# Kernel optimization log

Hardware: AMD Instinct MI355X
Metric: run time of the kernel (lower is better)

The kernel has to match this reference:

```python
import jax, jax.numpy as jnp
import numpy as np

B, N, K, F, S = 128, 116, 4, 72, 8
TOPK = 10
INTRA_T, INTER_T = 0.1, 0.2


def _safe_corr(f):
    # f: [batch, d, m] -> corr [batch, d, d], matching torch _safe_compute_correlation
    c = f - f.mean(axis=2, keepdims=True)
    cov = jnp.einsum('bim,bjm->bij', c, c)
    var = jnp.diagonal(cov, axis1=1, axis2=2)
    std = jnp.sqrt(jnp.clip(var, 1e-8, None))[:, :, None]
    corr = cov / (std * std.transpose(0, 2, 1) + 1e-8)
    return jnp.clip(corr, -1.0, 1.0)


def _sym(m):
    return (m + m.swapaxes(-1, -2)) * 0.5


def setup_inputs():
    key = jax.random.key(0)
    ks = jax.random.split(key, 8)
    def lin(k, out_d, in_d):
        return jax.random.normal(k, (out_d, in_d), jnp.float32) * (1.0 / np.sqrt(in_d))
    return {
        'band_features': jax.random.normal(ks[0], (B, N, K, F), jnp.float32),
        'attn_weights': jax.random.uniform(ks[1], (B, N, S, K), jnp.float32),
        'intra_thresh_adj': jnp.zeros((), jnp.float32),
        'inter_thresh_adj': jnp.zeros((), jnp.float32),
        'attn_fuse_weight': jnp.asarray(0.5, jnp.float32),
        'intra_W1': lin(ks[2], 64, N), 'intra_b1': jnp.zeros((64,), jnp.float32),
        'intra_W2': lin(ks[3], N, 64), 'intra_b2': jnp.zeros((N,), jnp.float32),
        'inter_W1': lin(ks[4], 32, K), 'inter_b1': jnp.zeros((32,), jnp.float32),
        'inter_W2': lin(ks[5], K, 32), 'inter_b2': jnp.zeros((K,), jnp.float32),
        'comp_W': lin(ks[6], 128, 2 * F + 6), 'comp_b': jnp.zeros((128,), jnp.float32),
    }


def reference(band_features, attn_weights, intra_thresh_adj, inter_thresh_adj,
              attn_fuse_weight, intra_W1, intra_b1, intra_W2, intra_b2,
              inter_W1, inter_b1, inter_W2, inter_b2, comp_W, comp_b):
    dt = band_features.dtype
    # ---- intra-band graph: [B*K, N, N] correlations ----
    x = band_features.transpose(0, 2, 1, 3).reshape(B * K, N, F)
    corr = _safe_corr(x)
    th = INTRA_T + jax.nn.sigmoid(intra_thresh_adj) * 0.2
    tmask = (jnp.abs(corr) > th).astype(dt)
    _, idx = jax.lax.top_k(jnp.abs(corr), min(TOPK, N))  # [B*K, N, k]
    bix = jnp.arange(B * K)[:, None, None]
    rix = jnp.arange(N)[None, :, None]
    kmask = jnp.zeros_like(corr).at[bix, rix, idx].set(1.0)
    sc = jax.nn.relu(_sym(corr * tmask * kmask))
    h = jax.nn.relu(sc.reshape(-1, N) @ intra_W1.T + intra_b1)  # dropout = eval identity
    intra = jax.nn.sigmoid(h @ intra_W2.T + intra_b2).reshape(B * K, N, N)
    intra_adj = _sym(intra).reshape(B, K, N, N)
    # ---- inter-band graph: [B*N, K, K] correlations ----
    y = band_features.reshape(B * N, K, F)
    base = _safe_corr(y)
    a = attn_weights.reshape(B * N, S, K).transpose(0, 2, 1)  # [B*N, K, S]
    acorr = _safe_corr(a)
    fw = jax.nn.sigmoid(attn_fuse_weight)
    base = fw * base + (1.0 - fw) * acorr
    th2 = INTER_T + jax.nn.sigmoid(inter_thresh_adj) * 0.2
    sc2 = jax.nn.relu(_sym(base * (jnp.abs(base) > th2).astype(dt)))
    h2 = jax.nn.relu(sc2.reshape(-1, K) @ inter_W1.T + inter_b1)
    inter = jax.nn.sigmoid(h2 @ inter_W2.T + inter_b2).reshape(B * N, K, K)
    inter_adj = _sym(inter).reshape(B, N, K, K)
    # ---- unified graph assembly (vectorized replacement of nested loops) ----
    kk = jnp.arange(K)
    bd = jnp.zeros((B, K, N, K, N), dt).at[:, kk, :, kk, :].set(
        intra_adj.transpose(1, 0, 2, 3))  # block-diagonal intra blocks
    unified = bd.reshape(B, K * N, K * N)
    kk1, kk2, nn = np.meshgrid(np.arange(K), np.arange(K), np.arange(N), indexing='ij')
    sel = (kk1 != kk2).ravel()
    k1f, k2f, nf = kk1.ravel()[sel], kk2.ravel()[sel], nn.ravel()[sel]
    vals = inter_adj[:, nf, k1f, k2f]  # [B, M]
    unified_adj = unified.at[:, k1f * N + nf, k2f * N + nf].set(vals)
    # ---- node features ----
    node_features = band_features.transpose(0, 2, 1, 3).reshape(B, K * N, F)
    # ---- graph-level features ----
    node_mean = band_features.mean(axis=(1, 2))
    node_std = jnp.std(band_features, axis=(1, 2), ddof=1)  # torch unbiased std
    deg = (intra_adj > 0).astype(dt).sum(axis=3)  # [B, K, N]
    tri = jnp.einsum('bkij,bkji->bki', intra_adj, intra_adj)  # diag of A@A
    clus = tri / (deg ** 2 + 1e-8)
    dens = (inter_adj > 0).astype(dt).mean(axis=(2, 3))  # [B, N]
    stren = inter_adj.mean(axis=(2, 3))
    gf = jnp.concatenate([
        node_mean, node_std,
        deg.mean(axis=(1, 2))[:, None], jnp.std(deg, axis=(1, 2), ddof=1)[:, None],
        clus.mean(axis=(1, 2))[:, None], jnp.std(clus, axis=(1, 2), ddof=1)[:, None],
        dens.mean(axis=1)[:, None], stren.mean(axis=1)[:, None]], axis=1)
    graph_features = jax.nn.relu(gf @ comp_W.T + comp_b)
    # ---- sparsity scalars ----
    intra_sp = 1.0 - (intra_adj > 0).astype(dt).mean()
    inter_sp = 1.0 - (inter_adj > 0).astype(dt).mean()
    it, jt = float(B * K * N * N), float(B * N * K * K)
    total_sp = (intra_sp * it + inter_sp * jt) / (it + jt)
    return (unified_adj, node_features, graph_features, intra_adj, inter_adj,
            intra_sp, inter_sp, total_sp)
```

## Files before the change

### kernel.cpp

```cpp
#include <hip/hip_runtime.h>
#include <math.h>

#define NB 128
#define NN_ 116
#define NK 4
#define NF 72
#define NS 8
#define TOPK 10

#define BK (NB*NK)
#define BN (NB*NN_)
#define NN2 (NN_*NN_)
#define KN (NK*NN_)
#define ROWS (BK*NN_)
#define LROW 117

#define OFF_UNI 0
#define SZ_UNI (NB*KN*KN)
#define OFF_NF (OFF_UNI + SZ_UNI)
#define SZ_NF (NB*KN*NF)
#define OFF_GF (OFF_NF + SZ_NF)
#define SZ_GF (NB*128)
#define OFF_IA (OFF_GF + SZ_GF)
#define SZ_IA (NB*NK*NN_*NN_)
#define OFF_IE (OFF_IA + SZ_IA)
#define SZ_IE (NB*NN_*NK*NK)
#define OFF_SP (OFF_IE + SZ_IE)

#define SCR_SC 0
#define SCR_CORR (SCR_SC + SZ_IA)
#define SCR_DEG (SCR_CORR + SZ_IA)
#define SCR_CLUS (SCR_DEG + ROWS)
#define SCR_DENS (SCR_CLUS + ROWS)
#define SCR_STREN (SCR_DENS + BN)
#define SCR_AUX (SCR_STREN + BN)

__device__ __forceinline__ float sigmoidf_(float x){ return 1.0f/(1.0f+expf(-x)); }
__device__ __forceinline__ float dot4_(float4 a, float4 b){
    return fmaf(a.x,b.x, fmaf(a.y,b.y, fmaf(a.z,b.z, a.w*b.w)));
}
#define CLIP1(x) fminf(1.0f, fmaxf(-1.0f, (x)))

__global__ __launch_bounds__(256, 1) void k_corr_inter(const float* __restrict__ band,
    const float* __restrict__ attn, const float* __restrict__ thadj2,
    const float* __restrict__ fwp,
    const float* __restrict__ eW1, const float* __restrict__ eb1,
    const float* __restrict__ eW2, const float* __restrict__ eb2,
    float* __restrict__ corr_out, float* __restrict__ inter_out,
    float* __restrict__ dens_out, float* __restrict__ stren_out)
{
    __shared__ float sx[NF*120];
    __shared__ float smu[120], srs[120];
    __shared__ float sW1[128], sb1[32], sW2[128], sb2[4];
    __shared__ float sMat[256*4];
    int t = threadIdx.x;
    if (blockIdx.x < 512){
        int bk = blockIdx.x;
        int b = bk >> 2, k = bk & 3;
        const float* xin = band + ((size_t)b*NN_*NK + k)*NF;
        for (int e = t; e < NN_*NF; e += 256){
            int n = e / NF, f = e - n*NF;
            sx[f*120 + n] = xin[(size_t)n*NK*NF + f];
        }
        for (int e = t; e < NF*4; e += 256)
            sx[(e>>2)*120 + NN_ + (e&3)] = 0.0f;
        __syncthreads();
        if (t < NN_){
            float s = 0.f, ss = 0.f;
            for (int f = 0; f < NF; ++f){ float v = sx[f*120+t]; s += v; ss += v*v; }
            float mu = s * (1.0f/NF);
            float sd = sqrtf(fmaxf(ss - s*mu, 1e-8f));
            smu[t] = mu; srs[t] = 1.0f/sd;
        }
        __syncthreads();
        for (int e = t; e < NF*NN_; e += 256){
            int f = e / NN_, n = e - f*NN_;
            sx[f*120+n] = (sx[f*120+n] - smu[n]) * srs[n];
        }
        __syncthreads();
        float* dst = corr_out + (size_t)bk * NN2;
        if (t < 225){
            int ti = t / 15, tj = t - ti*15;
            int i0 = ti*8, j0 = tj*8;
            float acc[8][8] = {};
            for (int f = 0; f < NF; ++f){
                const float4 a0 = *(const float4*)&sx[f*120 + i0];
                const float4 a1 = *(const float4*)&sx[f*120 + i0 + 4];
                const float4 c0 = *(const float4*)&sx[f*120 + j0];
                const float4 c1 = *(const float4*)&sx[f*120 + j0 + 4];
                float av[8] = {a0.x,a0.y,a0.z,a0.w,a1.x,a1.y,a1.z,a1.w};
                float cv[8] = {c0.x,c0.y,c0.z,c0.w,c1.x,c1.y,c1.z,c1.w};
                #pragma unroll
                for (int r = 0; r < 8; ++r)
                    #pragma unroll
                    for (int c = 0; c < 8; ++c)
                        acc[r][c] = fmaf(av[r], cv[c], acc[r][c]);
            }
            #pragma unroll
            for (int r = 0; r < 8; ++r){
                int i = i0 + r;
                if (i < NN_){
                    float4 v0;
                    v0.x = CLIP1(acc[r][0]); v0.y = CLIP1(acc[r][1]);
                    v0.z = CLIP1(acc[r][2]); v0.w = CLIP1(acc[r][3]);
                    *(float4*)&dst[i*NN_ + j0] = v0;
                    if (j0 + 4 <= 112){
                        float4 v1;
                        v1.x = CLIP1(acc[r][4]); v1.y = CLIP1(acc[r][5]);
                        v1.z = CLIP1(acc[r][6]); v1.w = CLIP1(acc[r][7]);
                        *(float4*)&dst[i*NN_ + j0 + 4] = v1;
                    }
                }
            }
        }
    } else {
        if (t < 128) sW1[t] = eW1[t];
        if (t < 32) sb1[t] = eb1[t];
        if (t >= 128 && t < 256) sW2[t-128] = eW2[t-128];
        if (t < 4) sb2[t] = eb2[t];
        __syncthreads();
        int l = t & 3;
        int il = t >> 2;
        size_t item = (size_t)(blockIdx.x - 512)*64 + il;

        const float* xr = band + item*(NK*NF) + l*NF;
        float s=0,p0=0,p1=0,p2=0,p3=0;
        for (int f = 0; f < NF; ++f){
            float v = xr[f];
            float v1=__shfl_xor(v,1), v2=__shfl_xor(v,2), v3=__shfl_xor(v,3);
            s += v; p0=fmaf(v,v,p0); p1=fmaf(v,v1,p1); p2=fmaf(v,v2,p2); p3=fmaf(v,v3,p3);
        }
        float mu = s*(1.0f/NF);
        float mu1=__shfl_xor(mu,1), mu2=__shfl_xor(mu,2), mu3=__shfl_xor(mu,3);
        float sd = sqrtf(fmaxf(p0 - s*mu, 1e-8f));
        float sd1=__shfl_xor(sd,1), sd2=__shfl_xor(sd,2), sd3=__shfl_xor(sd,3);
        float c0 = CLIP1((p0 - (float)NF*mu*mu )/(sd*sd +1e-8f));
        float c1 = CLIP1((p1 - (float)NF*mu*mu1)/(sd*sd1+1e-8f));
        float c2 = CLIP1((p2 - (float)NF*mu*mu2)/(sd*sd2+1e-8f));
        float c3 = CLIP1((p3 - (float)NF*mu*mu3)/(sd*sd3+1e-8f));

        const float* ar = attn + item*(NS*NK) + l;
        float as=0,q0=0,q1=0,q2=0,q3=0;
        #pragma unroll
        for (int s8 = 0; s8 < NS; ++s8){
            float v = ar[s8*NK];
            float v1=__shfl_xor(v,1), v2=__shfl_xor(v,2), v3=__shfl_xor(v,3);
            as += v; q0=fmaf(v,v,q0); q1=fmaf(v,v1,q1); q2=fmaf(v,v2,q2); q3=fmaf(v,v3,q3);
        }
        float am = as*(1.0f/NS);
        float am1=__shfl_xor(am,1), am2=__shfl_xor(am,2), am3=__shfl_xor(am,3);
        float ad = sqrtf(fmaxf(q0 - as*am, 1e-8f));
        float ad1=__shfl_xor(ad,1), ad2=__shfl_xor(ad,2), ad3=__shfl_xor(ad,3);
        float a0 = CLIP1((q0 - (float)NS*am*am )/(ad*ad +1e-8f));
        float a1 = CLIP1((q1 - (float)NS*am*am1)/(ad*ad1+1e-8f));
        float a2 = CLIP1((q2 - (float)NS*am*am2)/(ad*ad2+1e-8f));
        float a3 = CLIP1((q3 - (float)NS*am*am3)/(ad*ad3+1e-8f));

        float fwv = sigmoidf_(fwp[0]);
        float g0 = fwv*c0 + (1.0f-fwv)*a0;
        float g1 = fwv*c1 + (1.0f-fwv)*a1;
        float g2 = fwv*c2 + (1.0f-fwv)*a2;
        float g3 = fwv*c3 + (1.0f-fwv)*a3;
        float th2 = 0.2f + sigmoidf_(thadj2[0])*0.2f;
        float m0 = (fabsf(g0)>th2)?g0:0.f;
        float m1 = (fabsf(g1)>th2)?g1:0.f;
        float m2 = (fabsf(g2)>th2)?g2:0.f;
        float m3 = (fabsf(g3)>th2)?g3:0.f;

        sMat[il*16 + l*4 + (l^0)] = m0;
        sMat[il*16 + l*4 + (l^1)] = m1;
        sMat[il*16 + l*4 + (l^2)] = m2;
        sMat[il*16 + l*4 + (l^3)] = m3;
        __syncthreads();
        float x0 = fmaxf(0.5f*(sMat[il*16 + l*4 + 0] + sMat[il*16 + 0*4 + l]), 0.f);
        float x1 = fmaxf(0.5f*(sMat[il*16 + l*4 + 1] + sMat[il*16 + 1*4 + l]), 0.f);
        float x2 = fmaxf(0.5f*(sMat[il*16 + l*4 + 2] + sMat[il*16 + 2*4 + l]), 0.f);
        float x3 = fmaxf(0.5f*(sMat[il*16 + l*4 + 3] + sMat[il*16 + 3*4 + l]), 0.f);

        float h[32];
        #pragma unroll
        for (int o = 0; o < 32; ++o){
            float acc = sb1[o];
            acc = fmaf(sW1[o*4+0], x0, acc);
            acc = fmaf(sW1[o*4+1], x1, acc);
            acc = fmaf(sW1[o*4+2], x2, acc);
            acc = fmaf(sW1[o*4+3], x3, acc);
            h[o] = fmaxf(acc, 0.f);
        }
        float o0=sb2[0], o1=sb2[1], o2=sb2[2], o3=sb2[3];
        #pragma unroll
        for (int o = 0; o < 32; ++o){
            float hv = h[o];
            o0 = fmaf(sW2[0*32+o], hv, o0);
            o1 = fmaf(sW2[1*32+o], hv, o1);
            o2 = fmaf(sW2[2*32+o], hv, o2);
            o3 = fmaf(sW2[3*32+o], hv, o3);
        }
        o0 = sigmoidf_(o0); o1 = sigmoidf_(o1); o2 = sigmoidf_(o2); o3 = sigmoidf_(o3);
        __syncthreads();
        sMat[il*16 + l*4 + 0] = o0;
        sMat[il*16 + l*4 + 1] = o1;
        sMat[il*16 + l*4 + 2] = o2;
        sMat[il*16 + l*4 + 3] = o3;
        __syncthreads();
        float y0 = 0.5f*(o0 + sMat[il*16 + 0*4 + l]);
        float y1 = 0.5f*(o1 + sMat[il*16 + 1*4 + l]);
        float y2 = 0.5f*(o2 + sMat[il*16 + 2*4 + l]);
        float y3 = 0.5f*(o3 + sMat[il*16 + 3*4 + l]);
        *(float4*)&inter_out[item*16 + l*4] = make_float4(y0,y1,y2,y3);

        float cnt = ((y0>0.f)?1.f:0.f) + ((y1>0.f)?1.f:0.f) + ((y2>0.f)?1.f:0.f) + ((y3>0.f)?1.f:0.f);
        float sum = y0+y1+y2+y3;
        cnt += __shfl_xor(cnt,1); cnt += __shfl_xor(cnt,2);
        sum += __shfl_xor(sum,1); sum += __shfl_xor(sum,2);
        if (l == 0){
            dens_out[item]  = cnt * (1.0f/16.0f);
            stren_out[item] = sum * (1.0f/16.0f);
        }
    }
}

__global__ __launch_bounds__(512) void k_topk_mask(const float* __restrict__ corr_in,
    const float* __restrict__ thadj, float* __restrict__ sc_out)
{
    __shared__ float sc_[NN_*LROW];
    __shared__ unsigned skm[NN_*4];
    __shared__ unsigned stop[464*10];
    int bk = blockIdx.x;
    int t = threadIdx.x;
    const float* src = corr_in + (size_t)bk*NN2;
    for (int e = t; e < NN2; e += 512){
        int i = e / NN_, j = e - i*NN_;
        sc_[i*LROW + j] = src[e];
    }
    __syncthreads();
    if (t < NN_*4){
        int r = t >> 2, q = t & 3;
        const float* row = &sc_[r*LROW + q*29];
        int jbase = q*29;
        unsigned tv[TOPK];
        #pragma unroll
        for (int p = 0; p < TOPK; ++p) tv[p] = 0u;
        for (int jj = 0; jj < 29; ++jj){
            float c = fabsf(row[jj]);
            unsigned u = (__float_as_uint(c) & 0xFFFFFF80u) | (unsigned)(127 - (jbase + jj));
            #pragma unroll
            for (int p = 0; p < TOPK; ++p){
                unsigned old = tv[p];
                bool gt = u > old;
                tv[p] = gt ? u : old;
                u = gt ? old : u;
            }
        }
        #pragma unroll
        for (int p = 0; p < TOPK; ++p) stop[t*10 + p] = tv[p];
    }
    __syncthreads();
    if (t < NN_){
        const unsigned* L0 = &stop[(4*t+0)*10];
        const unsigned* L1 = &stop[(4*t+1)*10];
        const unsigned* L2 = &stop[(4*t+2)*10];
        const unsigned* L3 = &stop[(4*t+3)*10];
        int i0=0, i1=0, i2=0, i3=0;
        unsigned m0=0,m1=0,m2=0,m3=0;
        #pragma unroll
        for (int p = 0; p < TOPK; ++p){
            unsigned u0 = L0[i0], u1 = L1[i1], u2 = L2[i2], u3 = L3[i3];
            unsigned ua = u0 > u1 ? u0 : u1;
            unsigned ub = u2 > u3 ? u2 : u3;
            unsigned u  = ua > ub ? ua : ub;
            if (u == u0) ++i0; else if (u == u1) ++i1; else if (u == u2) ++i2; else ++i3;
            int j = 127 - (int)(u & 127u);
            unsigned bit = 1u << (j & 31);
            int w = j >> 5;
            if (w == 0) m0 |= bit; else if (w == 1) m1 |= bit; else if (w == 2) m2 |= bit; else m3 |= bit;
        }
        skm[t*4+0]=m0; skm[t*4+1]=m1; skm[t*4+2]=m2; skm[t*4+3]=m3;
    }
    __syncthreads();
    float th = 0.1f + sigmoidf_(thadj[0]) * 0.2f;
    float* dst = sc_out + (size_t)bk * NN2;
    for (int e = t; e < NN2; e += 512){
        int i = e / NN_, j = e - i*NN_;
        float cij = sc_[i*LROW + j];
        float cji = sc_[j*LROW + i];
        bool kij = (skm[i*4 + (j>>5)] >> (j&31)) & 1u;
        bool kji = (skm[j*4 + (i>>5)] >> (i&31)) & 1u;
        float mij = (fabsf(cij) > th && kij) ? cij : 0.0f;
        float mji = (fabsf(cji) > th && kji) ? cji : 0.0f;
        dst[e] = fmaxf(0.5f*(mij+mji), 0.0f);
    }
}

__global__ __launch_bounds__(256) void k_mlp(const float* __restrict__ sc,
    const float* __restrict__ W1, const float* __restrict__ b1,
    const float* __restrict__ W2, const float* __restrict__ b2,
    float* __restrict__ intra)
{
    __shared__ float sA_[14848];
    __shared__ float sH[64*68];
    __shared__ float sb1[64];
    __shared__ float sb2[128];
    int t = threadIdx.x;
    int r0 = blockIdx.x * 64;
    float* srow = sA_;
    float* sW1  = sA_ + 7424;
    for (int e4 = t; e4 < 1856; e4 += 256){
        *(float4*)&srow[e4*4] = *(const float4*)&sc[(size_t)r0*116 + e4*4];
        *(float4*)&sW1[e4*4]  = *(const float4*)&W1[e4*4];
    }
    if (t < 64) sb1[t] = b1[t];
    if (t < 128) sb2[t] = (t < NN_) ? b2[t] : 0.0f;
    __syncthreads();
    {
        int rg = t >> 4, og = t & 15;
        float acc[4][4] = {};
        for (int j4 = 0; j4 < 29; ++j4){
            float4 s[4], w[4];
            #pragma unroll
            for (int m = 0; m < 4; ++m) s[m] = *(const float4*)&srow[(rg+16*m)*116 + j4*4];
            #pragma unroll
            for (int n = 0; n < 4; ++n) w[n] = *(const float4*)&sW1[(og+16*n)*116 + j4*4];
            #pragma unroll
            for (int m = 0; m < 4; ++m)
                #pragma unroll
                for (int n = 0; n < 4; ++n)
                    acc[m][n] += dot4_(s[m], w[n]);
        }
        #pragma unroll
        for (int m = 0; m < 4; ++m)
            #pragma unroll
            for (int n = 0; n < 4; ++n)
                sH[(rg+16*m)*68 + og+16*n] = fmaxf(acc[m][n] + sb1[og+16*n], 0.0f);
    }
    __syncthreads();
    float* sW2 = sA_;
    for (int e = t; e < 128*64; e += 256){
        int j = e >> 6, o = e & 63;
        sW2[j*76 + o] = (j < NN_) ? W2[e] : 0.0f;
    }
    __syncthreads();
    {
        int rg = t >> 4, jg = t & 15;
        float acc[4][8] = {};
        for (int o4 = 0; o4 < 16; ++o4){
            float4 h[4], w[8];
            #pragma unroll
            for (int m = 0; m < 4; ++m) h[m] = *(const float4*)&sH[(rg+16*m)*68 + o4*4];
            #pragma unroll
            for (int q = 0; q < 8; ++q) w[q] = *(const float4*)&sW2[(jg+16*q)*76 + o4*4];
            #pragma unroll
            for (int m = 0; m < 4; ++m)
                #pragma unroll
                for (int q = 0; q < 8; ++q)
                    acc[m][q] += dot4_(h[m], w[q]);
        }
        #pragma unroll
        for (int m = 0; m < 4; ++m){
            int row = r0 + rg + 16*m;
            #pragma unroll
            for (int q = 0; q < 8; ++q){
                int j = jg + 16*q;
                if (j < NN_)
                    intra[(size_t)row*116 + j] = sigmoidf_(acc[m][q] + sb2[j]);
            }
        }
    }
}

__global__ __launch_bounds__(512) void k_sym_intra(const float* __restrict__ intra,
    float* __restrict__ intra_adj, float* __restrict__ deg_out, float* __restrict__ clus_out)
{
    __shared__ float sm[NN_*LROW];
    int bk = blockIdx.x, t = threadIdx.x;
    const float* src = intra + (size_t)bk*NN2;
    for (int e = t; e < NN2; e += 512){
        int i = e / NN_, j = e - i*NN_;
        sm[i*LROW + j] = src[e];
    }
    __syncthreads();
    float* dst = intra_adj + (size_t)bk*NN2;
    for (int e = t; e < NN2; e += 512){
        int i = e / NN_, j = e - i*NN_;
        dst[e] = 0.5f*(sm[i*LROW + j] + sm[j*LROW + i]);
    }
    if (t < NN_*4){
        int r = t >> 2, q = t & 3;
        float tri = 0.f, dg = 0.f;
        for (int jj = 0; jj < 29; ++jj){
            int j = q*29 + jj;
            float v = 0.5f*(sm[r*LROW+j] + sm[j*LROW+r]);
            tri = fmaf(v, v, tri);
            dg += (v > 0.f) ? 1.f : 0.f;
        }
        tri += __shfl_xor(tri,1); tri += __shfl_xor(tri,2);
        dg  += __shfl_xor(dg,1);  dg  += __shfl_xor(dg,2);
        if (q == 0){
            deg_out[(size_t)bk*NN_ + r]  = dg;
            clus_out[(size_t)bk*NN_ + r] = tri / (dg*dg + 1e-8f);
        }
    }
}

__global__ __launch_bounds__(256) void k_gstats_lin(const float* __restrict__ band,
    const float* __restrict__ deg, const float* __restrict__ clus,
    const float* __restrict__ dens, const float* __restrict__ stren,
    const float* __restrict__ Wc, const float* __restrict__ bc,
    float* __restrict__ gfo, float* __restrict__ aux)
{
    int b = blockIdx.x, t = threadIdx.x;
    __shared__ float sGf[152];
    __shared__ float sPs[18*14*4];
    __shared__ float sPq[18*14*4];
    __shared__ float sA[4], sB[4];

    if (t < 252){
        int fq = t % 18, g = t / 18;
        float4 s = make_float4(0,0,0,0), q = make_float4(0,0,0,0);
        const float* base = band + (size_t)b*(KN*NF);
        for (int nk = g; nk < KN; nk += 14){
            float4 v = *(const float4*)&base[nk*NF + fq*4];
            s.x += v.x; s.y += v.y; s.z += v.z; s.w += v.w;
            q.x = fmaf(v.x,v.x,q.x); q.y = fmaf(v.y,v.y,q.y);
            q.z = fmaf(v.z,v.z,q.z); q.w = fmaf(v.w,v.w,q.w);
        }
        int idx = (fq*14 + g)*4;
        *(float4*)&sPs[idx] = s;
        *(float4*)&sPq[idx] = q;
    }
    __syncthreads();
    if (t < NF){
        int fq = t >> 2, e = t & 3;
        float S = 0.f, Q = 0.f;
        for (int g = 0; g < 14; ++g){ S += sPs[(fq*14+g)*4+e]; Q += sPq[(fq*14+g)*4+e]; }
        float mean = S * (1.0f/(float)KN);
        float var = fmaxf((Q - S*mean)/((float)KN - 1.0f), 0.0f);
        sGf[t] = mean;
        sGf[NF + t] = sqrtf(var);
    }
    __syncthreads();

    float s = 0.f, ss = 0.f;
    for (int e = t; e < KN; e += 256){ float v = deg[(size_t)b*KN + e]; s += v; ss += v*v; }
    #pragma unroll
    for (int d = 1; d < 64; d <<= 1){ s += __shfl_xor(s,d); ss += __shfl_xor(ss,d); }
    if ((t & 63) == 0){ sA[t>>6] = s; sB[t>>6] = ss; }
    __syncthreads();
    if (t == 0){
        float S0 = sA[0]+sA[1]+sA[2]+sA[3], S1 = sB[0]+sB[1]+sB[2]+sB[3];
        float Mv = (float)KN, mean = S0/Mv;
        float var = fmaxf((S1 - S0*mean)/(Mv - 1.0f), 0.0f);
        sGf[144] = mean; sGf[145] = sqrtf(var);
        aux[b] = S0;
    }
    __syncthreads();

    s = 0.f; ss = 0.f;
    for (int e = t; e < KN; e += 256){ float v = clus[(size_t)b*KN + e]; s += v; ss += v*v; }
    #pragma unroll
    for (int d = 1; d < 64; d <<= 1){ s += __shfl_xor(s,d); ss += __shfl_xor(ss,d); }
    if ((t & 63) == 0){ sA[t>>6] = s; sB[t>>6] = ss; }
    __syncthreads();
    if (t == 0){
        float S0 = sA[0]+sA[1]+sA[2]+sA[3], S1 = sB[0]+sB[1]+sB[2]+sB[3];
        float Mv = (float)KN, mean = S0/Mv;
        float var = fmaxf((S1 - S0*mean)/(Mv - 1.0f), 0.0f);
        sGf[146] = mean; sGf[147] = sqrtf(var);
    }
    __syncthreads();

    s = 0.f; ss = 0.f;
    for (int e = t; e < NN_; e += 256){ s += dens[(size_t)b*NN_ + e]; ss += stren[(size_t)b*NN_ + e]; }
    #pragma unroll
    for (int d = 1; d < 64; d <<= 1){ s += __shfl_xor(s,d); ss += __shfl_xor(ss,d); }
    if ((t & 63) == 0){ sA[t>>6] = s; sB[t>>6] = ss; }
    __syncthreads();
    if (t == 0){
        float S0 = sA[0]+sA[1]+sA[2]+sA[3], S1 = sB[0]+sB[1]+sB[2]+sB[3];
        sGf[148] = S0 / (float)NN_;
        sGf[149] = S1 / (float)NN_;
        aux[128 + b] = S0 * 16.0f;
    }
    __syncthreads();

    if (t < 128){
        float acc = bc[t];
        const float* w = Wc + (size_t)t*150;
        for (int c = 0; c < 150; ++c) acc = fmaf(sGf[c], w[c], acc);
        gfo[(size_t)b*128 + t] = fmaxf(acc, 0.f);
    }
}

__global__ __launch_bounds__(128) void k_sparsity(const float* __restrict__ aux, float* __restrict__ out3)
{
    int t = threadIdx.x;
    float a = aux[t];
    float c = aux[128 + t];
    #pragma unroll
    for (int d = 1; d < 64; d <<= 1){ a += __shfl_xor(a,d); c += __shfl_xor(c,d); }
    __shared__ float sA[2], sC2[2];
    if ((t & 63) == 0){ sA[t>>6] = a; sC2[t>>6] = c; }
    __syncthreads();
    if (t == 0){
        float icnt = sA[0]+sA[1], jcnt = sC2[0]+sC2[1];
        const float it = 6889472.0f, jt = 237568.0f;
        float isp = 1.0f - icnt/it;
        float jsp = 1.0f - jcnt/jt;
        out3[0] = isp; out3[1] = jsp;
        out3[2] = (isp*it + jsp*jt)/(it + jt);
    }
}

#define UNQ (SZ_UNI/4)
#define NFQ (SZ_NF/4)
__global__ __launch_bounds__(256) void k_uninf(const float* __restrict__ intra_adj,
    const float* __restrict__ inter_adj, const float* __restrict__ band,
    float* __restrict__ uni, float* __restrict__ nf)
{
    int gid = blockIdx.x*256 + threadIdx.x;
    int gsz = gridDim.x*256;
    for (int q = gid; q < UNQ; q += gsz){
        int row = q / 116;
        int cq  = q - row*116;
        int b = row / KN;
        int p = row - b*KN;
        int k1 = p / NN_;
        int i  = p - k1*NN_;
        int k2 = cq / 29;
        int j0 = cq*4 - k2*NN_;
        float4 v;
        if (k2 == k1){
            v = *(const float4*)&intra_adj[(((size_t)b*NK + k1)*NN_ + i)*NN_ + j0];
        } else {
            int d = i - j0;
            float val = 0.f;
            if (d >= 0 && d < 4)
                val = inter_adj[(((size_t)b*NN_ + i)*NK + k1)*NK + k2];
            v.x = (d==0)?val:0.f;
            v.y = (d==1)?val:0.f;
            v.z = (d==2)?val:0.f;
            v.w = (d==3)?val:0.f;
        }
        *(float4*)&uni[(size_t)q*4] = v;
    }
    for (int q = gid; q < NFQ; q += gsz){
        int fq = q % 18;
        int rest = q / 18;
        int b = rest / KN;
        int p = rest - b*KN;
        int k = p / NN_;
        int n = p - k*NN_;
        float4 v = *(const float4*)&band[(((size_t)b*NN_ + n)*NK + k)*NF + fq*4];
        *(float4*)&nf[(size_t)q*4] = v;
    }
}

extern "C" void kernel_launch(void* const* d_in, const int* in_sizes, int n_in,
                              void* d_out, int out_size, void* d_ws, size_t ws_size,
                              hipStream_t stream)
{
    const float* band = (const float*)d_in[0];
    const float* attn = (const float*)d_in[1];
    const float* thA  = (const float*)d_in[2];
    const float* thE  = (const float*)d_in[3];
    const float* fw   = (const float*)d_in[4];
    const float* iW1  = (const float*)d_in[5];
    const float* ib1  = (const float*)d_in[6];
    const float* iW2  = (const float*)d_in[7];
    const float* ib2  = (const float*)d_in[8];
    const float* eW1  = (const float*)d_in[9];
    const float* eb1  = (const float*)d_in[10];
    const float* eW2  = (const float*)d_in[11];
    const float* eb2  = (const float*)d_in[12];
    const float* cW   = (const float*)d_in[13];
    const float* cb   = (const float*)d_in[14];

    float* out = (float*)d_out;
    float* uni = out + OFF_UNI;
    float* nf  = out + OFF_NF;
    float* gfo = out + OFF_GF;
    float* ia  = out + OFF_IA;
    float* ie  = out + OFF_IE;
    float* sp  = out + OFF_SP;

    float* scr_sc    = uni + SCR_SC;
    float* scr_corr  = uni + SCR_CORR;
    float* scr_deg   = uni + SCR_DEG;
    float* scr_clus  = uni + SCR_CLUS;
    float* scr_dens  = uni + SCR_DENS;
    float* scr_stren = uni + SCR_STREN;
    float* scr_aux   = uni + SCR_AUX;

    k_corr_inter<<<512 + BN/64, 256, 0, stream>>>(band, attn, thE, fw, eW1, eb1, eW2, eb2,
                                                  scr_corr, ie, scr_dens, scr_stren);
    k_topk_mask<<<BK, 512, 0, stream>>>(scr_corr, thA, scr_sc);
    k_mlp<<<ROWS/64, 256, 0, stream>>>(scr_sc, iW1, ib1, iW2, ib2, scr_sc);
    k_sym_intra<<<BK, 512, 0, stream>>>(scr_sc, ia, scr_deg, scr_clus);
    k_gstats_lin<<<NB, 256, 0, stream>>>(band, scr_deg, scr_clus, scr_dens, scr_stren,
                                         cW, cb, gfo, scr_aux);
    k_sparsity<<<1, 128, 0, stream>>>(scr_aux, sp);
    k_uninf<<<2048, 256, 0, stream>>>(ia, ie, band, uni, nf);
}
```

Measured before the change: 158.1 us.

## Fuse top-k masking into correlation kernel and merge symmetrize with graph stats

The correlation kernel now keeps the correlation tile in shared memory and runs the top-k selection, threshold and symmetrization in place, so the full correlation matrix no longer takes a round trip through global memory and one launch is gone. The symmetrize and graph-statistics kernels are merged into one per-batch kernel that loops over the four bands and keeps degree and clustering in shared memory. The sparsity reduction moves into the final kernel when workspace is available. The cost is more shared memory and lower parallelism: 128 blocks now do the symmetrize step instead of 512, and the top-k uses 2 threads per row instead of 4.

Measured after the change: 180.9 us. +14.4%, slower.

```diff
diff --git a/kernel.cpp b/kernel.cpp
--- a/kernel.cpp
+++ b/kernel.cpp
@@ -28,10 +28,7 @@
 #define OFF_SP (OFF_IE + SZ_IE)
 
 #define SCR_SC 0
-#define SCR_CORR (SCR_SC + SZ_IA)
-#define SCR_DEG (SCR_CORR + SZ_IA)
-#define SCR_CLUS (SCR_DEG + ROWS)
-#define SCR_DENS (SCR_CLUS + ROWS)
+#define SCR_DENS (SCR_SC + SZ_IA)
 #define SCR_STREN (SCR_DENS + BN)
 #define SCR_AUX (SCR_STREN + BN)
 
@@ -41,15 +38,18 @@
 }
 #define CLIP1(x) fminf(1.0f, fmaxf(-1.0f, (x)))
 
-__global__ __launch_bounds__(256, 1) void k_corr_inter(const float* __restrict__ band,
-    const float* __restrict__ attn, const float* __restrict__ thadj2,
-    const float* __restrict__ fwp,
+__global__ __launch_bounds__(256, 1) void k_front(const float* __restrict__ band,
+    const float* __restrict__ attn, const float* __restrict__ thadjA,
+    const float* __restrict__ thadjE, const float* __restrict__ fwp,
     const float* __restrict__ eW1, const float* __restrict__ eb1,
     const float* __restrict__ eW2, const float* __restrict__ eb2,
-    float* __restrict__ corr_out, float* __restrict__ inter_out,
+    float* __restrict__ sc_out, float* __restrict__ inter_out,
     float* __restrict__ dens_out, float* __restrict__ stren_out)
 {
     __shared__ float sx[NF*120];
+    __shared__ float sC[NN_*LROW];
+    __shared__ unsigned stop[232*10];
+    __shared__ unsigned skm[NN_*4];
     __shared__ float smu[120], srs[120];
     __shared__ float sW1[128], sb1[32], sW2[128], sb2[4];
     __shared__ float sMat[256*4];
@@ -78,7 +78,6 @@
             sx[f*120+n] = (sx[f*120+n] - smu[n]) * srs[n];
         }
         __syncthreads();
-        float* dst = corr_out + (size_t)bk * NN2;
         if (t < 225){
             int ti = t / 15, tj = t - ti*15;
             int i0 = ti*8, j0 = tj*8;
@@ -100,18 +99,66 @@
             for (int r = 0; r < 8; ++r){
                 int i = i0 + r;
                 if (i < NN_){
-                    float4 v0;
-                    v0.x = CLIP1(acc[r][0]); v0.y = CLIP1(acc[r][1]);
-                    v0.z = CLIP1(acc[r][2]); v0.w = CLIP1(acc[r][3]);
-                    *(float4*)&dst[i*NN_ + j0] = v0;
-                    if (j0 + 4 <= 112){
-                        float4 v1;
-                        v1.x = CLIP1(acc[r][4]); v1.y = CLIP1(acc[r][5]);
-                        v1.z = CLIP1(acc[r][6]); v1.w = CLIP1(acc[r][7]);
-                        *(float4*)&dst[i*NN_ + j0 + 4] = v1;
+                    #pragma unroll
+                    for (int c = 0; c < 8; ++c){
+                        int j = j0 + c;
+                        if (j < NN_) sC[i*LROW + j] = CLIP1(acc[r][c]);
                     }
                 }
             }
+        }
+        __syncthreads();
+        if (t < 232){
+            int r = t >> 1, h = t & 1;
+            const float* row = &sC[r*LROW + h*58];
+            int jbase = h*58;
+            unsigned tv[TOPK];
+            #pragma unroll
+            for (int p = 0; p < TOPK; ++p) tv[p] = 0u;
+            for (int jj = 0; jj < 58; ++jj){
+                float c = fabsf(row[jj]);
+                unsigned u = (__float_as_uint(c) & 0xFFFFFF80u) | (unsigned)(127 - (jbase + jj));
+                #pragma unroll
+                for (int p = 0; p < TOPK; ++p){
+                    unsigned old = tv[p];
+                    bool gt = u > old;
+                    tv[p] = gt ? u : old;
+                    u = gt ? old : u;
+                }
+            }
+            #pragma unroll
+            for (int p = 0; p < TOPK; ++p) stop[t*10 + p] = tv[p];
+        }
+        __syncthreads();
+        if (t < NN_){
+            const unsigned* A = &stop[(2*t)*10];
+            const unsigned* Bp = &stop[(2*t+1)*10];
+            int pa = 0, pb = 0;
+            unsigned m0=0,m1=0,m2=0,m3=0;
+            #pragma unroll
+            for (int p = 0; p < TOPK; ++p){
+                unsigned ua = A[pa], ub = Bp[pb];
+                unsigned u;
+                if (ua > ub){ u = ua; ++pa; } else { u = ub; ++pb; }
+                int j = 127 - (int)(u & 127u);
+                unsigned bit = 1u << (j & 31);
+                int w = j >> 5;
+                if (w == 0) m0 |= bit; else if (w == 1) m1 |= bit; else if (w == 2) m2 |= bit; else m3 |= bit;
+            }
+            skm[t*4+0]=m0; skm[t*4+1]=m1; skm[t*4+2]=m2; skm[t*4+3]=m3;
+        }
+        __syncthreads();
+        float th = 0.1f + sigmoidf_(thadjA[0]) * 0.2f;
+        float* dst = sc_out + (size_t)bk * NN2;
+        for (int e = t; e < NN2; e += 256){
+            int i = e / NN_, j = e - i*NN_;
+            float cij = sC[i*LROW + j];
+            float cji = sC[j*LROW + i];
+            bool kij = (skm[i*4 + (j>>5)] >> (j&31)) & 1u;
+            bool kji = (skm[j*4 + (i>>5)] >> (i&31)) & 1u;
+            float mij = (fabsf(cij) > th && kij) ? cij : 0.0f;
+            float mji = (fabsf(cji) > th && kji) ? cji : 0.0f;
+            dst[e] = fmaxf(0.5f*(mij+mji), 0.0f);
         }
     } else {
         if (t < 128) sW1[t] = eW1[t];
@@ -161,7 +208,7 @@
         float g1 = fwv*c1 + (1.0f-fwv)*a1;
         float g2 = fwv*c2 + (1.0f-fwv)*a2;
         float g3 = fwv*c3 + (1.0f-fwv)*a3;
-        float th2 = 0.2f + sigmoidf_(thadj2[0])*0.2f;
+        float th2 = 0.2f + sigmoidf_(thadjE[0])*0.2f;
         float m0 = (fabsf(g0)>th2)?g0:0.f;
         float m1 = (fabsf(g1)>th2)?g1:0.f;
         float m2 = (fabsf(g2)>th2)?g2:0.f;
@@ -217,78 +264,6 @@
             dens_out[item]  = cnt * (1.0f/16.0f);
             stren_out[item] = sum * (1.0f/16.0f);
         }
-    }
-}
-
-__global__ __launch_bounds__(512) void k_topk_mask(const float* __restrict__ corr_in,
-    const float* __restrict__ thadj, float* __restrict__ sc_out)
-{
-    __shared__ float sc_[NN_*LROW];
-    __shared__ unsigned skm[NN_*4];
-    __shared__ unsigned stop[464*10];
-    int bk = blockIdx.x;
-    int t = threadIdx.x;
-    const float* src = corr_in + (size_t)bk*NN2;
-    for (int e = t; e < NN2; e += 512){
-        int i = e / NN_, j = e - i*NN_;
-        sc_[i*LROW + j] = src[e];
-    }
-    __syncthreads();
-    if (t < NN_*4){
-        int r = t >> 2, q = t & 3;
-        const float* row = &sc_[r*LROW + q*29];
-        int jbase = q*29;
-        unsigned tv[TOPK];
-        #pragma unroll
-        for (int p = 0; p < TOPK; ++p) tv[p] = 0u;
-        for (int jj = 0; jj < 29; ++jj){
-            float c = fabsf(row[jj]);
-            unsigned u = (__float_as_uint(c) & 0xFFFFFF80u) | (unsigned)(127 - (jbase + jj));
-            #pragma unroll
-            for (int p = 0; p < TOPK; ++p){
-                unsigned old = tv[p];
-                bool gt = u > old;
-                tv[p] = gt ? u : old;
-                u = gt ? old : u;
-            }
-        }
-        #pragma unroll
-        for (int p = 0; p < TOPK; ++p) stop[t*10 + p] = tv[p];
-    }
-    __syncthreads();
-    if (t < NN_){
-        const unsigned* L0 = &stop[(4*t+0)*10];
-        const unsigned* L1 = &stop[(4*t+1)*10];
-        const unsigned* L2 = &stop[(4*t+2)*10];
-        const unsigned* L3 = &stop[(4*t+3)*10];
-        int i0=0, i1=0, i2=0, i3=0;
-        unsigned m0=0,m1=0,m2=0,m3=0;
-        #pragma unroll
-        for (int p = 0; p < TOPK; ++p){
-            unsigned u0 = L0[i0], u1 = L1[i1], u2 = L2[i2], u3 = L3[i3];
-            unsigned ua = u0 > u1 ? u0 : u1;
-            unsigned ub = u2 > u3 ? u2 : u3;
-            unsigned u  = ua > ub ? ua : ub;
-            if (u == u0) ++i0; else if (u == u1) ++i1; else if (u == u2) ++i2; else ++i3;
-            int j = 127 - (int)(u & 127u);
-            unsigned bit = 1u << (j & 31);
-            int w = j >> 5;
-            if (w == 0) m0 |= bit; else if (w == 1) m1 |= bit; else if (w == 2) m2 |= bit; else m3 |= bit;
-        }
-        skm[t*4+0]=m0; skm[t*4+1]=m1; skm[t*4+2]=m2; skm[t*4+3]=m3;
-    }
-    __syncthreads();
-    float th = 0.1f + sigmoidf_(thadj[0]) * 0.2f;
-    float* dst = sc_out + (size_t)bk * NN2;
-    for (int e = t; e < NN2; e += 512){
-        int i = e / NN_, j = e - i*NN_;
-        float cij = sc_[i*LROW + j];
-        float cji = sc_[j*LROW + i];
-        bool kij = (skm[i*4 + (j>>5)] >> (j&31)) & 1u;
-        bool kji = (skm[j*4 + (i>>5)] >> (i&31)) & 1u;
-        float mij = (fabsf(cij) > th && kij) ? cij : 0.0f;
-        float mji = (fabsf(cji) > th && kji) ? cji : 0.0f;
-        dst[e] = fmaxf(0.5f*(mij+mji), 0.0f);
     }
 }
 
@@ -368,51 +343,49 @@
     }
 }
 
-__global__ __launch_bounds__(512) void k_sym_intra(const float* __restrict__ intra,
-    float* __restrict__ intra_adj, float* __restrict__ deg_out, float* __restrict__ clus_out)
+__global__ __launch_bounds__(512) void k_symg(const float* __restrict__ intra,
+    const float* __restrict__ dens, const float* __restrict__ stren,
+    const float* __restrict__ band, const float* __restrict__ Wc,
+    const float* __restrict__ bc, float* __restrict__ ia,
+    float* __restrict__ gfo, float* __restrict__ aux)
 {
     __shared__ float sm[NN_*LROW];
-    int bk = blockIdx.x, t = threadIdx.x;
-    const float* src = intra + (size_t)bk*NN2;
-    for (int e = t; e < NN2; e += 512){
-        int i = e / NN_, j = e - i*NN_;
-        sm[i*LROW + j] = src[e];
-    }
-    __syncthreads();
-    float* dst = intra_adj + (size_t)bk*NN2;
-    for (int e = t; e < NN2; e += 512){
-        int i = e / NN_, j = e - i*NN_;
-        dst[e] = 0.5f*(sm[i*LROW + j] + sm[j*LROW + i]);
-    }
-    if (t < NN_*4){
-        int r = t >> 2, q = t & 3;
-        float tri = 0.f, dg = 0.f;
-        for (int jj = 0; jj < 29; ++jj){
-            int j = q*29 + jj;
-            float v = 0.5f*(sm[r*LROW+j] + sm[j*LROW+r]);
-            tri = fmaf(v, v, tri);
-            dg += (v > 0.f) ? 1.f : 0.f;
-        }
-        tri += __shfl_xor(tri,1); tri += __shfl_xor(tri,2);
-        dg  += __shfl_xor(dg,1);  dg  += __shfl_xor(dg,2);
-        if (q == 0){
-            deg_out[(size_t)bk*NN_ + r]  = dg;
-            clus_out[(size_t)bk*NN_ + r] = tri / (dg*dg + 1e-8f);
-        }
-    }
-}
-
-__global__ __launch_bounds__(256) void k_gstats_lin(const float* __restrict__ band,
-    const float* __restrict__ deg, const float* __restrict__ clus,
-    const float* __restrict__ dens, const float* __restrict__ stren,
-    const float* __restrict__ Wc, const float* __restrict__ bc,
-    float* __restrict__ gfo, float* __restrict__ aux)
-{
+    __shared__ float sdeg[KN], sclus[KN];
+    __shared__ float sPs[18*14*4], sPq[18*14*4];
+    __shared__ float sGf[152];
+    __shared__ float sA[8], sB[8];
     int b = blockIdx.x, t = threadIdx.x;
-    __shared__ float sGf[152];
-    __shared__ float sPs[18*14*4];
-    __shared__ float sPq[18*14*4];
-    __shared__ float sA[4], sB[4];
+
+    for (int k = 0; k < NK; ++k){
+        const float* src = intra + ((size_t)(b*NK + k))*NN2;
+        for (int e = t; e < NN2; e += 512){
+            int i = e / NN_, j = e - i*NN_;
+            sm[i*LROW + j] = src[e];
+        }
+        __syncthreads();
+        float* dst = ia + ((size_t)(b*NK + k))*NN2;
+        for (int e = t; e < NN2; e += 512){
+            int i = e / NN_, j = e - i*NN_;
+            dst[e] = 0.5f*(sm[i*LROW + j] + sm[j*LROW + i]);
+        }
+        if (t < NN_*4){
+            int r = t >> 2, q = t & 3;
+            float tri = 0.f, dg = 0.f;
+            for (int jj = 0; jj < 29; ++jj){
+                int j = q*29 + jj;
+                float v = 0.5f*(sm[r*LROW+j] + sm[j*LROW+r]);
+                tri = fmaf(v, v, tri);
+                dg += (v > 0.f) ? 1.f : 0.f;
+            }
+            tri += __shfl_xor(tri,1); tri += __shfl_xor(tri,2);
+            dg  += __shfl_xor(dg,1);  dg  += __shfl_xor(dg,2);
+            if (q == 0){
+                sdeg[k*NN_ + r]  = dg;
+                sclus[k*NN_ + r] = tri / (dg*dg + 1e-8f);
+            }
+        }
+        __syncthreads();
+    }
 
     if (t < 252){
         int fq = t % 18, g = t / 18;
@@ -440,14 +413,16 @@
     }
     __syncthreads();
 
-    float s = 0.f, ss = 0.f;
-    for (int e = t; e < KN; e += 256){ float v = deg[(size_t)b*KN + e]; s += v; ss += v*v; }
+    float s = (t < KN) ? sdeg[t] : 0.f;
+    float ss = s*s;
     #pragma unroll
     for (int d = 1; d < 64; d <<= 1){ s += __shfl_xor(s,d); ss += __shfl_xor(ss,d); }
     if ((t & 63) == 0){ sA[t>>6] = s; sB[t>>6] = ss; }
     __syncthreads();
     if (t == 0){
-        float S0 = sA[0]+sA[1]+sA[2]+sA[3], S1 = sB[0]+sB[1]+sB[2]+sB[3];
+        float S0=0.f, S1=0.f;
+        #pragma unroll
+        for (int w = 0; w < 8; ++w){ S0 += sA[w]; S1 += sB[w]; }
         float Mv = (float)KN, mean = S0/Mv;
         float var = fmaxf((S1 - S0*mean)/(Mv - 1.0f), 0.0f);
         sGf[144] = mean; sGf[145] = sqrtf(var);
@@ -455,28 +430,32 @@
     }
     __syncthreads();
 
-    s = 0.f; ss = 0.f;
-    for (int e = t; e < KN; e += 256){ float v = clus[(size_t)b*KN + e]; s += v; ss += v*v; }
+    s = (t < KN) ? sclus[t] : 0.f;
+    ss = s*s;
     #pragma unroll
     for (int d = 1; d < 64; d <<= 1){ s += __shfl_xor(s,d); ss += __shfl_xor(ss,d); }
     if ((t & 63) == 0){ sA[t>>6] = s; sB[t>>6] = ss; }
     __syncthreads();
     if (t == 0){
-        float S0 = sA[0]+sA[1]+sA[2]+sA[3], S1 = sB[0]+sB[1]+sB[2]+sB[3];
+        float S0=0.f, S1=0.f;
+        #pragma unroll
+        for (int w = 0; w < 8; ++w){ S0 += sA[w]; S1 += sB[w]; }
         float Mv = (float)KN, mean = S0/Mv;
         float var = fmaxf((S1 - S0*mean)/(Mv - 1.0f), 0.0f);
         sGf[146] = mean; sGf[147] = sqrtf(var);
     }
     __syncthreads();
 
-    s = 0.f; ss = 0.f;
-    for (int e = t; e < NN_; e += 256){ s += dens[(size_t)b*NN_ + e]; ss += stren[(size_t)b*NN_ + e]; }
+    s = (t < NN_) ? dens[(size_t)b*NN_ + t] : 0.f;
+    ss = (t < NN_) ? stren[(size_t)b*NN_ + t] : 0.f;
     #pragma unroll
     for (int d = 1; d < 64; d <<= 1){ s += __shfl_xor(s,d); ss += __shfl_xor(ss,d); }
     if ((t & 63) == 0){ sA[t>>6] = s; sB[t>>6] = ss; }
     __syncthreads();
     if (t == 0){
-        float S0 = sA[0]+sA[1]+sA[2]+sA[3], S1 = sB[0]+sB[1]+sB[2]+sB[3];
+        float S0=0.f, S1=0.f;
+        #pragma unroll
+        for (int w = 0; w < 8; ++w){ S0 += sA[w]; S1 += sB[w]; }
         sGf[148] = S0 / (float)NN_;
         sGf[149] = S1 / (float)NN_;
         aux[128 + b] = S0 * 16.0f;
@@ -491,21 +470,17 @@
     }
 }
 
-__global__ __launch_bounds__(128) void k_sparsity(const float* __restrict__ aux, float* __restrict__ out3)
+__global__ __launch_bounds__(64) void k_sparsity(const float* __restrict__ aux, float* __restrict__ out3)
 {
     int t = threadIdx.x;
-    float a = aux[t];
-    float c = aux[128 + t];
+    float a = aux[t] + aux[64 + t];
+    float c = aux[128 + t] + aux[192 + t];
     #pragma unroll
     for (int d = 1; d < 64; d <<= 1){ a += __shfl_xor(a,d); c += __shfl_xor(c,d); }
-    __shared__ float sA[2], sC2[2];
-    if ((t & 63) == 0){ sA[t>>6] = a; sC2[t>>6] = c; }
-    __syncthreads();
     if (t == 0){
-        float icnt = sA[0]+sA[1], jcnt = sC2[0]+sC2[1];
         const float it = 6889472.0f, jt = 237568.0f;
-        float isp = 1.0f - icnt/it;
-        float jsp = 1.0f - jcnt/jt;
+        float isp = 1.0f - a/it;
+        float jsp = 1.0f - c/jt;
         out3[0] = isp; out3[1] = jsp;
         out3[2] = (isp*it + jsp*jt)/(it + jt);
     }
@@ -515,8 +490,23 @@
 #define NFQ (SZ_NF/4)
 __global__ __launch_bounds__(256) void k_uninf(const float* __restrict__ intra_adj,
     const float* __restrict__ inter_adj, const float* __restrict__ band,
-    float* __restrict__ uni, float* __restrict__ nf)
+    const float* __restrict__ aux, float* __restrict__ uni, float* __restrict__ nf,
+    float* __restrict__ sp, int do_sp)
 {
+    if (do_sp && blockIdx.x == 0 && threadIdx.x < 64){
+        int t = threadIdx.x;
+        float a = aux[t] + aux[64 + t];
+        float c = aux[128 + t] + aux[192 + t];
+        #pragma unroll
+        for (int d = 1; d < 64; d <<= 1){ a += __shfl_xor(a,d); c += __shfl_xor(c,d); }
+        if (t == 0){
+            const float it = 6889472.0f, jt = 237568.0f;
+            float isp = 1.0f - a/it;
+            float jsp = 1.0f - c/jt;
+            sp[0] = isp; sp[1] = jsp;
+            sp[2] = (isp*it + jsp*jt)/(it + jt);
+        }
+    }
     int gid = blockIdx.x*256 + threadIdx.x;
     int gsz = gridDim.x*256;
     for (int q = gid; q < UNQ; q += gsz){
@@ -584,20 +574,19 @@
     float* sp  = out + OFF_SP;
 
     float* scr_sc    = uni + SCR_SC;
-    float* scr_corr  = uni + SCR_CORR;
-    float* scr_deg   = uni + SCR_DEG;
-    float* scr_clus  = uni + SCR_CLUS;
     float* scr_dens  = uni + SCR_DENS;
     float* scr_stren = uni + SCR_STREN;
-    float* scr_aux   = uni + SCR_AUX;
-
-    k_corr_inter<<<512 + BN/64, 256, 0, stream>>>(band, attn, thE, fw, eW1, eb1, eW2, eb2,
-                                                  scr_corr, ie, scr_dens, scr_stren);
-    k_topk_mask<<<BK, 512, 0, stream>>>(scr_corr, thA, scr_sc);
+
+    int ws_ok = (ws_size >= 256*sizeof(float));
+    float* aux = ws_ok ? (float*)d_ws : (uni + SCR_AUX);
+
+    k_front<<<512 + BN/64, 256, 0, stream>>>(band, attn, thA, thE, fw,
+                                             eW1, eb1, eW2, eb2,
+                                             scr_sc, ie, scr_dens, scr_stren);
     k_mlp<<<ROWS/64, 256, 0, stream>>>(scr_sc, iW1, ib1, iW2, ib2, scr_sc);
-    k_sym_intra<<<BK, 512, 0, stream>>>(scr_sc, ia, scr_deg, scr_clus);
-    k_gstats_lin<<<NB, 256, 0, stream>>>(band, scr_deg, scr_clus, scr_dens, scr_stren,
-                                         cW, cb, gfo, scr_aux);
-    k_sparsity<<<1, 128, 0, stream>>>(scr_aux, sp);
-    k_uninf<<<2048, 256, 0, stream>>>(ia, ie, band, uni, nf);
-}
+    k_symg<<<NB, 512, 0, stream>>>(scr_sc, scr_dens, scr_stren, band, cW, cb,
+                                   ia, gfo, aux);
+    if (!ws_ok)
+        k_sparsity<<<1, 64, 0, stream>>>(aux, sp);
+    k_uninf<<<2048, 256, 0, stream>>>(ia, ie, band, aux, uni, nf, sp, ws_ok ? 1 : 0);
+}
```

## Fold node-feature copy into first kernel and sparsity reduction into final kernel

Applied to the files above, without the earlier changes.

Moves the band-to-node_features copy out of the final unified-adjacency kernel into extra blocks of the first correlation/inter kernel, so it overlaps with the correlation work. When the workspace is large enough, the aux counts go to d_ws and the sparsity reduction runs inside the last kernel, which removes one tiny launch. The first kernel gets extra blocks, and the fused sparsity path depends on the workspace size.

Result: faster. 153.1 us (-3.1%).

```diff
diff --git a/kernel.cpp b/kernel.cpp
--- a/kernel.cpp
+++ b/kernel.cpp
@@ -35,6 +35,12 @@
 #define SCR_STREN (SCR_DENS + BN)
 #define SCR_AUX (SCR_STREN + BN)
 
+#define NFQ (SZ_NF/4)
+#define UNQ (SZ_UNI/4)
+#define NB_CORR 512
+#define NB_INTER (BN/64)
+#define NB_COPY 1044
+
 __device__ __forceinline__ float sigmoidf_(float x){ return 1.0f/(1.0f+expf(-x)); }
 __device__ __forceinline__ float dot4_(float4 a, float4 b){
     return fmaf(a.x,b.x, fmaf(a.y,b.y, fmaf(a.z,b.z, a.w*b.w)));
@@ -47,14 +53,15 @@
     const float* __restrict__ eW1, const float* __restrict__ eb1,
     const float* __restrict__ eW2, const float* __restrict__ eb2,
     float* __restrict__ corr_out, float* __restrict__ inter_out,
-    float* __restrict__ dens_out, float* __restrict__ stren_out)
+    float* __restrict__ dens_out, float* __restrict__ stren_out,
+    float* __restrict__ nf)
 {
     __shared__ float sx[NF*120];
     __shared__ float smu[120], srs[120];
     __shared__ float sW1[128], sb1[32], sW2[128], sb2[4];
     __shared__ float sMat[256*4];
     int t = threadIdx.x;
-    if (blockIdx.x < 512){
+    if (blockIdx.x < NB_CORR){
         int bk = blockIdx.x;
         int b = bk >> 2, k = bk & 3;
         const float* xin = band + ((size_t)b*NN_*NK + k)*NF;
@@ -113,7 +120,7 @@
                 }
             }
         }
-    } else {
+    } else if (blockIdx.x < NB_CORR + NB_INTER){
         if (t < 128) sW1[t] = eW1[t];
         if (t < 32) sb1[t] = eb1[t];
         if (t >= 128 && t < 256) sW2[t-128] = eW2[t-128];
@@ -121,7 +128,7 @@
         __syncthreads();
         int l = t & 3;
         int il = t >> 2;
-        size_t item = (size_t)(blockIdx.x - 512)*64 + il;
+        size_t item = (size_t)(blockIdx.x - NB_CORR)*64 + il;
 
         const float* xr = band + item*(NK*NF) + l*NF;
         float s=0,p0=0,p1=0,p2=0,p3=0;
@@ -217,6 +224,19 @@
             dens_out[item]  = cnt * (1.0f/16.0f);
             stren_out[item] = sum * (1.0f/16.0f);
         }
+    } else {
+        int gid = (blockIdx.x - NB_CORR - NB_INTER)*256 + t;
+        int gsz = NB_COPY*256;
+        for (int q = gid; q < NFQ; q += gsz){
+            int fq = q % 18;
+            int rest = q / 18;
+            int b = rest / KN;
+            int p = rest - b*KN;
+            int k = p / NN_;
+            int n = p - k*NN_;
+            float4 v = *(const float4*)&band[(((size_t)b*NN_ + n)*NK + k)*NF + fq*4];
+            *(float4*)&nf[(size_t)q*4] = v;
+        }
     }
 }
 
@@ -491,32 +511,40 @@
     }
 }
 
-__global__ __launch_bounds__(128) void k_sparsity(const float* __restrict__ aux, float* __restrict__ out3)
+__global__ __launch_bounds__(64) void k_sparsity(const float* __restrict__ aux, float* __restrict__ out3)
 {
     int t = threadIdx.x;
-    float a = aux[t];
-    float c = aux[128 + t];
+    float a = aux[t] + aux[64 + t];
+    float c = aux[128 + t] + aux[192 + t];
     #pragma unroll
     for (int d = 1; d < 64; d <<= 1){ a += __shfl_xor(a,d); c += __shfl_xor(c,d); }
-    __shared__ float sA[2], sC2[2];
-    if ((t & 63) == 0){ sA[t>>6] = a; sC2[t>>6] = c; }
-    __syncthreads();
     if (t == 0){
-        float icnt = sA[0]+sA[1], jcnt = sC2[0]+sC2[1];
         const float it = 6889472.0f, jt = 237568.0f;
-        float isp = 1.0f - icnt/it;
-        float jsp = 1.0f - jcnt/jt;
+        float isp = 1.0f - a/it;
+        float jsp = 1.0f - c/jt;
         out3[0] = isp; out3[1] = jsp;
         out3[2] = (isp*it + jsp*jt)/(it + jt);
     }
 }
 
-#define UNQ (SZ_UNI/4)
-#define NFQ (SZ_NF/4)
 __global__ __launch_bounds__(256) void k_uninf(const float* __restrict__ intra_adj,
-    const float* __restrict__ inter_adj, const float* __restrict__ band,
-    float* __restrict__ uni, float* __restrict__ nf)
-{
+    const float* __restrict__ inter_adj, const float* __restrict__ aux,
+    float* __restrict__ uni, float* __restrict__ sp, int do_sp)
+{
+    if (do_sp && blockIdx.x == 0 && threadIdx.x < 64){
+        int t = threadIdx.x;
+        float a = aux[t] + aux[64 + t];
+        float c = aux[128 + t] + aux[192 + t];
+        #pragma unroll
+        for (int d = 1; d < 64; d <<= 1){ a += __shfl_xor(a,d); c += __shfl_xor(c,d); }
+        if (t == 0){
+            const float it = 6889472.0f, jt = 237568.0f;
+            float isp = 1.0f - a/it;
+            float jsp = 1.0f - c/jt;
+            sp[0] = isp; sp[1] = jsp;
+            sp[2] = (isp*it + jsp*jt)/(it + jt);
+        }
+    }
     int gid = blockIdx.x*256 + threadIdx.x;
     int gsz = gridDim.x*256;
     for (int q = gid; q < UNQ; q += gsz){
@@ -543,16 +571,6 @@
         }
         *(float4*)&uni[(size_t)q*4] = v;
     }
-    for (int q = gid; q < NFQ; q += gsz){
-        int fq = q % 18;
-        int rest = q / 18;
-        int b = rest / KN;
-        int p = rest - b*KN;
-        int k = p / NN_;
-        int n = p - k*NN_;
-        float4 v = *(const float4*)&band[(((size_t)b*NN_ + n)*NK + k)*NF + fq*4];
-        *(float4*)&nf[(size_t)q*4] = v;
-    }
 }
 
 extern "C" void kernel_launch(void* const* d_in, const int* in_sizes, int n_in,
@@ -589,15 +607,19 @@
     float* scr_clus  = uni + SCR_CLUS;
     float* scr_dens  = uni + SCR_DENS;
     float* scr_stren = uni + SCR_STREN;
-    float* scr_aux   = uni + SCR_AUX;
-
-    k_corr_inter<<<512 + BN/64, 256, 0, stream>>>(band, attn, thE, fw, eW1, eb1, eW2, eb2,
-                                                  scr_corr, ie, scr_dens, scr_stren);
+
+    int ws_ok = (ws_size >= 256*sizeof(float));
+    float* aux = ws_ok ? (float*)d_ws : (uni + SCR_AUX);
+
+    k_corr_inter<<<NB_CORR + NB_INTER + NB_COPY, 256, 0, stream>>>(
+        band, attn, thE, fw, eW1, eb1, eW2, eb2,
+        scr_corr, ie, scr_dens, scr_stren, nf);
     k_topk_mask<<<BK, 512, 0, stream>>>(scr_corr, thA, scr_sc);
     k_mlp<<<ROWS/64, 256, 0, stream>>>(scr_sc, iW1, ib1, iW2, ib2, scr_sc);
     k_sym_intra<<<BK, 512, 0, stream>>>(scr_sc, ia, scr_deg, scr_clus);
     k_gstats_lin<<<NB, 256, 0, stream>>>(band, scr_deg, scr_clus, scr_dens, scr_stren,
-                                         cW, cb, gfo, scr_aux);
-    k_sparsity<<<1, 128, 0, stream>>>(scr_aux, sp);
-    k_uninf<<<2048, 256, 0, stream>>>(ia, ie, band, uni, nf);
-}
+                                         cW, cb, gfo, aux);
+    if (!ws_ok)
+        k_sparsity<<<1, 64, 0, stream>>>(aux, sp);
+    k_uninf<<<2048, 256, 0, stream>>>(ia, ie, aux, uni, sp, ws_ok ? 1 : 0);
+}
```
